# Performance work log

Measured on AMD Instinct MI355X. Metric: run time of the kernel, lower is better.

## Reference

```python
import jax, jax.numpy as jnp
import numpy as np

EPS = 1e-5
HID = 32
FUSED = 33 * 33 * 33  # 35937


def _subnet(x, gamma, beta, W1, b1, W2, b2, W3, b3):
    # BatchNorm1d in training mode: batch mean / biased variance
    mu = jnp.mean(x, axis=0)
    var = jnp.mean((x - mu) ** 2, axis=0)
    xn = (x - mu) / jnp.sqrt(var + EPS) * gamma + beta
    h = jax.nn.relu(xn @ W1 + b1)
    h = jax.nn.relu(h @ W2 + b2)
    return jax.nn.relu(h @ W3 + b3)


def _subnet_params(key, in_dim):
    ks = jax.random.split(key, 6)
    s_in = 1.0 / np.sqrt(in_dim)
    s_h = 1.0 / np.sqrt(HID)
    return dict(
        gamma=jnp.ones((in_dim,), jnp.float32),
        beta=jnp.zeros((in_dim,), jnp.float32),
        W1=jax.random.uniform(ks[0], (in_dim, HID), jnp.float32, -s_in, s_in),
        b1=jax.random.uniform(ks[1], (HID,), jnp.float32, -s_in, s_in),
        W2=jax.random.uniform(ks[2], (HID, HID), jnp.float32, -s_h, s_h),
        b2=jax.random.uniform(ks[3], (HID,), jnp.float32, -s_h, s_h),
        W3=jax.random.uniform(ks[4], (HID, HID), jnp.float32, -s_h, s_h),
        b3=jax.random.uniform(ks[5], (HID,), jnp.float32, -s_h, s_h),
    )


def setup_inputs() -> dict:
    key = jax.random.key(0)
    ks = jax.random.split(key, 10)
    B = 8192
    inp = {
        'US_x': jax.random.normal(ks[0], (B, 1024), jnp.float32),
        'CDFI_x': jax.random.normal(ks[1], (B, 1024), jnp.float32),
        'marker_x': jax.random.normal(ks[2], (B, 10), jnp.float32),
    }
    for pref, k, d in (('us', ks[3], 1024), ('cd', ks[4], 1024), ('mk', ks[5], 10)):
        for n, v in _subnet_params(k, d).items():
            inp[f'{pref}_{n}'] = v
    s1 = 1.0 / np.sqrt(FUSED)
    s2 = 1.0 / np.sqrt(33)
    inp['Wf1'] = jax.random.uniform(ks[6], (FUSED, 33), jnp.float32, -s1, s1)
    inp['bf1'] = jax.random.uniform(ks[7], (33,), jnp.float32, -s1, s1)
    inp['Wf2'] = jax.random.uniform(ks[8], (33, 5), jnp.float32, -s2, s2)
    inp['bf2'] = jax.random.uniform(ks[9], (5,), jnp.float32, -s2, s2)
    return inp


def reference(US_x, CDFI_x, marker_x,
              us_gamma, us_beta, us_W1, us_b1, us_W2, us_b2, us_W3, us_b3,
              cd_gamma, cd_beta, cd_W1, cd_b1, cd_W2, cd_b2, cd_W3, cd_b3,
              mk_gamma, mk_beta, mk_W1, mk_b1, mk_W2, mk_b2, mk_W3, mk_b3,
              Wf1, bf1, Wf2, bf2):
    B = US_x.shape[0]
    us_h = _subnet(US_x, us_gamma, us_beta, us_W1, us_b1, us_W2, us_b2, us_W3, us_b3)
    cd_h = _subnet(CDFI_x, cd_gamma, cd_beta, cd_W1, cd_b1, cd_W2, cd_b2, cd_W3, cd_b3)
    mk_h = _subnet(marker_x, mk_gamma, mk_beta, mk_W1, mk_b1, mk_W2, mk_b2, mk_W3, mk_b3)
    ones = jnp.ones((B, 1), jnp.float32)
    us1 = jnp.concatenate([ones, us_h], axis=1)   # [B,33]
    cd1 = jnp.concatenate([ones, cd_h], axis=1)   # [B,33]
    mk1 = jnp.concatenate([ones, mk_h], axis=1)   # [B,33]
    # fused[b,k,j,i] = mk1[b,k] * cd1[b,j] * us1[b,i]; flattened row-major
    fused = jnp.einsum('bk,bj,bi->bkji', mk1, cd1, us1).reshape(B, FUSED)
    h = jax.nn.relu(fused @ Wf1 + bf1)
    return jax.nn.sigmoid(h @ Wf2 + bf2)
```

## Files before the change

kernel.cpp:

```cpp
#include <hip/hip_runtime.h>
#include <hip/hip_bf16.h>
#include <math.h>

typedef __hip_bfloat16 bf16;
typedef __attribute__((ext_vector_type(4))) float f32x4;
typedef __attribute__((ext_vector_type(8))) short s16x8;

#define NB 8192
#define KP 1152
#define NP 1152
#define NK 36
#define SBLK 256

struct SubP {
    const float* x; const float* gamma; const float* beta;
    const float* W1; const float* b1; const float* W2; const float* b2;
    const float* W3; const float* b3;
    float* sum; float* sumsq; float* a; float* b1p; float* hout;
    int F;
};
struct SubP3 { SubP s[3]; };

__global__ void __launch_bounds__(256) stats3_kernel(SubP3 P) {
    const SubP p = P.s[blockIdx.z];
    int t = threadIdx.x;
    int blk = blockIdx.x;
    int row0 = blk * 32;
    if (p.F == 1024) {
        f32x4 s = {0.f, 0.f, 0.f, 0.f}, s2 = {0.f, 0.f, 0.f, 0.f};
        const float* xp = p.x + (size_t)row0 * 1024 + t * 4;
        #pragma unroll 8
        for (int r = 0; r < 32; r++) {
            f32x4 v = *(const f32x4*)(xp + (size_t)r * 1024);
            s += v; s2 += v * v;
        }
        int f = t * 4;
        *(f32x4*)&p.sum[(size_t)blk * 2048 + f]   = s;
        *(f32x4*)&p.sumsq[(size_t)blk * 2048 + f] = s2;
    } else {
        __shared__ float ls[16], ls2[16];
        if (t < 16) { ls[t] = 0.f; ls2[t] = 0.f; }
        __syncthreads();
        int F = p.F;
        for (int idx = t; idx < 32 * F; idx += 256) {
            float v = p.x[(size_t)row0 * F + idx];
            int f = idx % 10;
            atomicAdd(&ls[f], v);
            atomicAdd(&ls2[f], v * v);
        }
        __syncthreads();
        if (t < F) {
            p.sum[(size_t)blk * 2048 + t]   = ls[t];
            p.sumsq[(size_t)blk * 2048 + t] = ls2[t];
        }
    }
}

__global__ void prep3_kernel(SubP3 P) {
    const SubP p = P.s[blockIdx.y];
    int f0 = blockIdx.x * 32;
    if (f0 >= p.F) return;
    int t = threadIdx.x;
    __shared__ float c_sh[32];
    __shared__ float red[8][33];
    __shared__ float rs[8][33], rs2[8][33];
    int fc = p.F - f0; if (fc > 32) fc = 32;
    int fi = t & 31, g = t >> 5;
    {
        float s = 0.f, s2 = 0.f;
        if (fi < fc) {
            for (int blk = g; blk < SBLK; blk += 8) {
                s  += p.sum[(size_t)blk * 2048 + f0 + fi];
                s2 += p.sumsq[(size_t)blk * 2048 + f0 + fi];
            }
        }
        rs[g][fi] = s; rs2[g][fi] = s2;
    }
    __syncthreads();
    if (t < 32) {
        float c = 0.f;
        if (t < fc) {
            float sm = 0.f, sq = 0.f;
            #pragma unroll
            for (int gg = 0; gg < 8; gg++) { sm += rs[gg][t]; sq += rs2[gg][t]; }
            int f = f0 + t;
            float mu  = sm * (1.f / 8192.f);
            float var = sq * (1.f / 8192.f) - mu * mu;
            float a = p.gamma[f] * rsqrtf(var + 1e-5f);
            p.a[f] = a;
            c = p.beta[f] - mu * a;
        }
        c_sh[t] = c;
    }
    __syncthreads();
    int h = t & 31; g = t >> 5;
    float s = 0.f;
    for (int fi2 = g; fi2 < fc; fi2 += 8)
        s += c_sh[fi2] * p.W1[(size_t)(f0 + fi2) * 32 + h];
    red[g][h] = s;
    __syncthreads();
    if (t < 32) {
        float tot = 0.f;
        #pragma unroll
        for (int gg = 0; gg < 8; gg++) tot += red[gg][t];
        atomicAdd(&p.b1p[t], tot);
    }
}

__global__ void __launch_bounds__(256) subnet3_kernel(SubP3 P) {
    const SubP p = P.s[blockIdx.y];
    const int F = p.F;
    __shared__ float smem[8832];
    float* Red = smem;
    float* H1  = smem + 3456;
    float* W23 = smem + 4608;
    float* H2  = smem;

    int t = threadIdx.x;
    int row0 = blockIdx.x * 32;
    int kg = t >> 6;
    int lane = t & 63;
    int hg = lane & 7, h0 = hg * 4;
    int rg = (lane >> 3) & 3;
    int ks = lane >> 5;

    float acc[4][8] = {};

    if (F == 1024) {
        float* Xt = smem;
        float* Wt = smem + 4224;
        int xr = t >> 3, xc = (t & 7) * 16;
        int wk = t >> 1, wh = (t & 1) * 16;
        const float* xbase = p.x + (size_t)row0 * 1024;
        f32x4 xp[4], wp[4]; float av;
        #pragma unroll
        for (int i = 0; i < 4; i++) xp[i] = *(const f32x4*)&xbase[(size_t)xr * 1024 + xc + i * 4];
        #pragma unroll
        for (int i = 0; i < 4; i++) wp[i] = *(const f32x4*)&p.W1[(size_t)wk * 32 + wh + i * 4];
        av = p.a[wk];
        int kb = (kg * 2 + ks) * 16;
        for (int c = 0; c < 8; c++) {
            __syncthreads();
            #pragma unroll
            for (int i = 0; i < 4; i++) *(f32x4*)&Xt[xr * 132 + xc + i * 4] = xp[i];
            #pragma unroll
            for (int i = 0; i < 4; i++) *(f32x4*)&Wt[wk * 36 + wh + i * 4] = wp[i] * av;
            if (c < 7) {
                int k0 = (c + 1) * 128;
                #pragma unroll
                for (int i = 0; i < 4; i++) xp[i] = *(const f32x4*)&xbase[(size_t)xr * 1024 + k0 + xc + i * 4];
                #pragma unroll
                for (int i = 0; i < 4; i++) wp[i] = *(const f32x4*)&p.W1[(size_t)(k0 + wk) * 32 + wh + i * 4];
                av = p.a[k0 + wk];
            }
            __syncthreads();
            #pragma unroll
            for (int s = 0; s < 4; s++) {
                int kk = kb + s * 4;
                f32x4 wv[4], xv[8];
                #pragma unroll
                for (int j = 0; j < 4; j++)  wv[j]  = *(const f32x4*)&Wt[(kk + j) * 36 + h0];
                #pragma unroll
                for (int ri = 0; ri < 8; ri++) xv[ri] = *(const f32x4*)&Xt[(rg + 4 * ri) * 132 + kk];
                #pragma unroll
                for (int j = 0; j < 4; j++)
                    #pragma unroll
                    for (int hi = 0; hi < 4; hi++) {
                        float w = wv[j][hi];
                        #pragma unroll
                        for (int ri = 0; ri < 8; ri++)
                            acc[hi][ri] = fmaf(w, xv[ri][j], acc[hi][ri]);
                    }
            }
        }
    } else {
        float* Xt = smem;
        float* Wt = smem + 2176;
        int kbase = (kg * 2 + ks) * 8;
        for (int k0 = 0; k0 < F; k0 += 64) {
            int kc = F - k0; if (kc > 64) kc = 64;
            int kcp = (kc + 3) & ~3;
            __syncthreads();
            for (int idx = t; idx < 32 * kcp; idx += 256) {
                int r = idx / kcp, kk = idx - r * kcp;
                Xt[r * 68 + kk] = (kk < kc) ? p.x[(size_t)(row0 + r) * F + k0 + kk] : 0.f;
            }
            for (int idx = t; idx < kcp * 32; idx += 256) {
                int kk = idx >> 5, hh = idx & 31;
                Wt[kk * 36 + hh] = (kk < kc) ? p.a[k0 + kk] * p.W1[(size_t)(k0 + kk) * 32 + hh] : 0.f;
            }
            __syncthreads();
            #pragma unroll
            for (int s = 0; s < 2; s++) {
                int kk = kbase + s * 4;
                if (kk < kcp) {
                    f32x4 wv[4], xv[8];
                    #pragma unroll
                    for (int j = 0; j < 4; j++)  wv[j]  = *(const f32x4*)&Wt[(kk + j) * 36 + h0];
                    #pragma unroll
                    for (int ri = 0; ri < 8; ri++) xv[ri] = *(const f32x4*)&Xt[(rg + 4 * ri) * 68 + kk];
                    #pragma unroll
                    for (int j = 0; j < 4; j++)
                        #pragma unroll
                        for (int hi = 0; hi < 4; hi++) {
                            float w = wv[j][hi];
                            #pragma unroll
                            for (int ri = 0; ri < 8; ri++)
                                acc[hi][ri] = fmaf(w, xv[ri][j], acc[hi][ri]);
                        }
                }
            }
        }
    }
    #pragma unroll
    for (int hi = 0; hi < 4; hi++)
        #pragma unroll
        for (int ri = 0; ri < 8; ri++)
            acc[hi][ri] += __shfl_xor(acc[hi][ri], 32);
    __syncthreads();
    if (kg > 0 && ks == 0) {
        #pragma unroll
        for (int ri = 0; ri < 8; ri++) {
            int r = rg + 4 * ri;
            f32x4 v = {acc[0][ri], acc[1][ri], acc[2][ri], acc[3][ri]};
            *(f32x4*)&Red[(kg - 1) * 1152 + r * 36 + h0] = v;
        }
    }
    for (int idx = t; idx < 1024; idx += 256) W23[(idx >> 5) * 33 + (idx & 31)] = p.W2[idx];
    __syncthreads();
    if (kg == 0 && ks == 0) {
        f32x4 b;
        #pragma unroll
        for (int hi = 0; hi < 4; hi++) b[hi] = p.b1[h0 + hi] + p.b1p[h0 + hi];
        #pragma unroll
        for (int ri = 0; ri < 8; ri++) {
            int r = rg + 4 * ri;
            f32x4 v = {acc[0][ri], acc[1][ri], acc[2][ri], acc[3][ri]};
            #pragma unroll
            for (int pp = 0; pp < 3; pp++)
                v += *(const f32x4*)&Red[pp * 1152 + r * 36 + h0];
            v += b;
            #pragma unroll
            for (int hi = 0; hi < 4; hi++)
                H1[r * 36 + h0 + hi] = fmaxf(v[hi], 0.f);
        }
    }
    __syncthreads();
    int h = t & 31, rq = t >> 5;
    {
        float a2[4] = {};
        for (int q = 0; q < 32; q++) {
            float w = W23[q * 33 + h];
            #pragma unroll
            for (int i = 0; i < 4; i++) a2[i] += H1[(rq * 4 + i) * 36 + q] * w;
        }
        float bv = p.b2[h];
        #pragma unroll
        for (int i = 0; i < 4; i++) H2[(rq * 4 + i) * 36 + h] = fmaxf(a2[i] + bv, 0.f);
    }
    __syncthreads();
    for (int idx = t; idx < 1024; idx += 256) W23[(idx >> 5) * 33 + (idx & 31)] = p.W3[idx];
    __syncthreads();
    {
        float a3[4] = {};
        for (int q = 0; q < 32; q++) {
            float w = W23[q * 33 + h];
            #pragma unroll
            for (int i = 0; i < 4; i++) a3[i] += H2[(rq * 4 + i) * 36 + q] * w;
        }
        float bv = p.b3[h];
        #pragma unroll
        for (int i = 0; i < 4; i++)
            p.hout[(size_t)(row0 + rq * 4 + i) * 32 + h] = fmaxf(a3[i] + bv, 0.f);
    }
}

__global__ void __launch_bounds__(256) build_both(const float* __restrict__ mk_h,
                           const float* __restrict__ us_h,
                           bf16* __restrict__ p1,
                           const float* __restrict__ Wf1, bf16* __restrict__ W2t) {
    int blk = blockIdx.x;
    int t = threadIdx.x;
    if (blk < NB / 4) {
        int r = t >> 6, lane = t & 63;
        int b = blk * 4 + r;
        __shared__ float mk1[4][34], us1[4][34];
        if (lane == 0) { mk1[r][0] = 1.f; us1[r][0] = 1.f; }
        if (lane < 32) mk1[r][lane + 1] = mk_h[(size_t)b * 32 + lane];
        else           us1[r][lane - 31] = us_h[(size_t)b * 32 + (lane - 32)];
        __syncthreads();
        #pragma unroll
        for (int c = 0; c < 3; c++) {
            int chunk = lane + 64 * c;
            if (chunk < 144) {
                int base = chunk * 8;
                s16x8 v;
                #pragma unroll
                for (int e = 0; e < 8; e++) {
                    int idx = base + e;
                    float val = 0.f;
                    if (idx < 1089) {
                        int k = idx / 33, i = idx - k * 33;
                        val = mk1[r][k] * us1[r][i];
                    }
                    __hip_bfloat16 hb = __float2bfloat16(val);
                    v[e] = *(short*)&hb;
                }
                *(s16x8*)(p1 + (size_t)b * KP + base) = v;
            }
        }
    } else {
        int kj = blk - NB / 4;
        int k = kj / 33, j = kj - k * 33;
        __shared__ float tile[1089];
        const float* src = Wf1 + (size_t)k * 35937 + (size_t)j * 1089;
        for (int idx = t; idx < 1089; idx += 256) tile[idx] = src[idx];
        __syncthreads();
        for (int idx = t; idx < 1089; idx += 256) {
            int o = idx / 33, i = idx - o * 33;
            W2t[(size_t)(j * 33 + o) * KP + k * 33 + i] = __float2bfloat16(tile[i * 33 + o]);
        }
        if (k == 0) {
            bf16 z = __float2bfloat16(0.f);
            for (int idx = t; idx < 33 * 63; idx += 256) {
                int o = idx / 63, kkp = 1089 + idx - o * 63;
                W2t[(size_t)(j * 33 + o) * KP + kkp] = z;
            }
        }
    }
}

__global__ void __launch_bounds__(256) gemm_kernel(const bf16* __restrict__ A,
                                                   const bf16* __restrict__ Bt,
                                                   bf16* __restrict__ S) {
    __shared__ __align__(16) bf16 As[2][128 * 32];
    __shared__ __align__(16) bf16 Bs[2][128 * 32];
    int t = threadIdx.x;
    int m0 = blockIdx.x * 128;
    int n0 = blockIdx.y * 128;
    int wave = t >> 6, lane = t & 63;
    int wm = (wave & 1) * 64, wn = (wave >> 1) * 64;
    int fr = lane & 15;
    int q  = lane >> 4;
    int rsw = (fr >> 1) & 3;

    int lr = lane >> 2;
    int sslot = (lane & 3) ^ ((lane >> 3) & 3);
    const bf16* Ag = A  + (size_t)(m0 + wave * 32 + lr) * KP + sslot * 8;
    const bf16* Bg = Bt + (size_t)(n0 + wave * 32 + lr) * KP + sslot * 8;

    f32x4 acc[4][4] = {};

    auto stage = [&](int buf, int k0) {
        bf16* Ad = &As[buf][wave * 1024];
        bf16* Bd = &Bs[buf][wave * 1024];
        __builtin_amdgcn_global_load_lds(
            (const __attribute__((address_space(1))) void*)(Ag + k0),
            (__attribute__((address_space(3))) void*)(Ad), 16, 0, 0);
        __builtin_amdgcn_global_load_lds(
            (const __attribute__((address_space(1))) void*)(Ag + k0 + (size_t)16 * KP),
            (__attribute__((address_space(3))) void*)(Ad + 16 * 32), 16, 0, 0);
        __builtin_amdgcn_global_load_lds(
            (const __attribute__((address_space(1))) void*)(Bg + k0),
            (__attribute__((address_space(3))) void*)(Bd), 16, 0, 0);
        __builtin_amdgcn_global_load_lds(
            (const __attribute__((address_space(1))) void*)(Bg + k0 + (size_t)16 * KP),
            (__attribute__((address_space(3))) void*)(Bd + 16 * 32), 16, 0, 0);
    };

    stage(0, 0);
    __syncthreads();
    int cur = 0;
    for (int ks = 0; ks < NK; ks++) {
        if (ks < NK - 1) stage(cur ^ 1, (ks + 1) * 32);
        const bf16* Ab = &As[cur][0];
        const bf16* Bb = &Bs[cur][0];
        s16x8 bfr[4];
        #pragma unroll
        for (int nt = 0; nt < 4; nt++) {
            int row = wn + nt * 16 + fr;
            bfr[nt] = *(const s16x8*)(Bb + row * 32 + ((q ^ rsw) * 8));
        }
        #pragma unroll
        for (int mt = 0; mt < 4; mt++) {
            int row = wm + mt * 16 + fr;
            s16x8 af = *(const s16x8*)(Ab + row * 32 + ((q ^ rsw) * 8));
            #pragma unroll
            for (int nt = 0; nt < 4; nt++)
                acc[mt][nt] = __builtin_amdgcn_mfma_f32_16x16x32_bf16(af, bfr[nt], acc[mt][nt], 0, 0, 0);
        }
        __syncthreads();
        cur ^= 1;
    }
    int col = lane & 15, rowg = (lane >> 4) * 4;
    #pragma unroll
    for (int mt = 0; mt < 4; mt++)
        #pragma unroll
        for (int nt = 0; nt < 4; nt++)
            #pragma unroll
            for (int r = 0; r < 4; r++) {
                int gr = m0 + wm + mt * 16 + rowg + r;
                int gc = n0 + wn + nt * 16 + col;
                S[(size_t)gr * NP + gc] = __float2bfloat16(acc[mt][nt][r]);
            }
}

__global__ void __launch_bounds__(256) epilogue_kernel(const bf16* __restrict__ S,
                                const float* __restrict__ cd_h,
                                const float* __restrict__ bf1, const float* __restrict__ Wf2,
                                const float* __restrict__ bf2, float* __restrict__ out) {
    int w = threadIdx.x >> 6;
    int lane = threadIdx.x & 63;
    int b = blockIdx.x * 4 + w;
    __shared__ __align__(16) unsigned short Sl[4][1152];
    __shared__ float cdsh[4][33];
    __shared__ float hsh[4][40];
    const bf16* Srow = S + (size_t)b * NP;
    #pragma unroll
    for (int pass = 0; pass < 3; pass++) {
        int idx = lane + pass * 64;
        if (idx < 144)
            *(s16x8*)&Sl[w][idx * 8] = *(const s16x8*)(Srow + idx * 8);
    }
    if (lane == 0) cdsh[w][0] = 1.f;
    if (lane < 32) cdsh[w][lane + 1] = cd_h[(size_t)b * 32 + lane];
    __syncthreads();
    if (lane < 33) {
        float acc = bf1[lane];
        #pragma unroll 3
        for (int j = 0; j < 33; j++) {
            unsigned short sv = Sl[w][j * 33 + lane];
            acc += cdsh[w][j] * __bfloat162float(*(bf16*)&sv);
        }
        hsh[w][lane] = fmaxf(acc, 0.f);
    }
    __syncthreads();
    if (lane < 5) {
        float o = bf2[lane];
        for (int q = 0; q < 33; q++) o += hsh[w][q] * Wf2[q * 5 + lane];
        out[(size_t)b * 5 + lane] = 1.f / (1.f + expf(-o));
    }
}

extern "C" void kernel_launch(void* const* d_in, const int* in_sizes, int n_in,
                              void* d_out, int out_size, void* d_ws, size_t ws_size,
                              hipStream_t stream) {
    const float* US_x     = (const float*)d_in[0];
    const float* CDFI_x   = (const float*)d_in[1];
    const float* marker_x = (const float*)d_in[2];
    const float* Wf1      = (const float*)d_in[27];
    const float* bf1      = (const float*)d_in[28];
    const float* Wf2      = (const float*)d_in[29];
    const float* bf2      = (const float*)d_in[30];
    float* out = (float*)d_out;

    char* ws = (char*)d_ws;
    size_t off = 0;
    auto alloc = [&](size_t bytes) -> void* {
        void* p = ws + off;
        off = (off + bytes + 255) & ~(size_t)255;
        return p;
    };

    float* b1p_buf  = (float*)alloc(3 * 128 * sizeof(float));
    float* pstat    = (float*)alloc((size_t)3 * SBLK * 2048 * sizeof(float));
    float* a_buf[3], *h_buf[3];
    for (int i = 0; i < 3; i++) {
        a_buf[i] = (float*)alloc(1024 * 4);
        h_buf[i] = (float*)alloc((size_t)NB * 32 * 4);
    }
    bf16*  p1   = (bf16*)alloc((size_t)NB * KP * 2);
    bf16*  W2t  = (bf16*)alloc((size_t)NP * KP * 2);
    bf16*  S    = (bf16*)alloc((size_t)NB * NP * 2);

    SubP3 P;
    const float* xs[3] = {US_x, CDFI_x, marker_x};
    int Fs[3] = {1024, 1024, 10};
    for (int i = 0; i < 3; i++) {
        int base = 3 + i * 8;
        P.s[i].x     = xs[i];
        P.s[i].gamma = (const float*)d_in[base + 0];
        P.s[i].beta  = (const float*)d_in[base + 1];
        P.s[i].W1    = (const float*)d_in[base + 2];
        P.s[i].b1    = (const float*)d_in[base + 3];
        P.s[i].W2    = (const float*)d_in[base + 4];
        P.s[i].b2    = (const float*)d_in[base + 5];
        P.s[i].W3    = (const float*)d_in[base + 6];
        P.s[i].b3    = (const float*)d_in[base + 7];
        P.s[i].sum   = pstat + (size_t)i * SBLK * 2048;
        P.s[i].sumsq = pstat + (size_t)i * SBLK * 2048 + 1024;
        P.s[i].b1p   = b1p_buf + i * 128;
        P.s[i].a     = a_buf[i];
        P.s[i].hout  = h_buf[i];
        P.s[i].F     = Fs[i];
    }

    float* us_h = h_buf[0];
    float* cd_h = h_buf[1];
    float* mk_h = h_buf[2];

    hipMemsetAsync(b1p_buf, 0, 3 * 128 * sizeof(float), stream);

    stats3_kernel<<<dim3(SBLK, 1, 3), 256, 0, stream>>>(P);
    prep3_kernel<<<dim3(32, 3), 256, 0, stream>>>(P);
    subnet3_kernel<<<dim3(256, 3), 256, 0, stream>>>(P);

    build_both<<<NB / 4 + 1089, 256, 0, stream>>>(mk_h, us_h, p1, Wf1, W2t);

    gemm_kernel<<<dim3(NB / 128, NP / 128), 256, 0, stream>>>(p1, W2t, S);

    epilogue_kernel<<<NB / 4, 256, 0, stream>>>(S, cd_h, bf1, Wf2, bf2, out);
}
```

Baseline: 255.0 us.

## Restructure bf16 GEMM to 256x144 tiles with 8 waves and split-phase prefetch

The GEMM block tile grows from 128x128 with 4 waves to 256x144 with 8 waves, and the K step from 32 to 64. Each wave now owns 32 rows across all 144 columns, so every loaded B fragment is reused over two A fragments. The next A tile is prefetched before the first K half and the next B tile between the two halves, with explicit vmcnt waits and raw barriers in place of __syncthreads. MFMA sections run at raised s_setprio. This gives more reuse per LDS load and fewer barriers, at the cost of 112KB of LDS (one block per CU) and heavier register use from 18 accumulators plus 9 B fragments.

Measured after the change: 246.4 us. -3.4%, faster.

```diff
diff --git a/kernel.cpp b/kernel.cpp
--- a/kernel.cpp
+++ b/kernel.cpp
@@ -9,7 +9,7 @@
 #define NB 8192
 #define KP 1152
 #define NP 1152
-#define NK 36
+#define NKT 18
 #define SBLK 256
 
 struct SubP {
@@ -330,78 +330,108 @@
     }
 }
 
-__global__ void __launch_bounds__(256) gemm_kernel(const bf16* __restrict__ A,
+__global__ void __launch_bounds__(512) gemm_kernel(const bf16* __restrict__ A,
                                                    const bf16* __restrict__ Bt,
                                                    bf16* __restrict__ S) {
-    __shared__ __align__(16) bf16 As[2][128 * 32];
-    __shared__ __align__(16) bf16 Bs[2][128 * 32];
+    __shared__ __align__(16) bf16 As[2][256 * 64];
+    __shared__ __align__(16) bf16 Bs[2][192 * 64];
     int t = threadIdx.x;
-    int m0 = blockIdx.x * 128;
-    int n0 = blockIdx.y * 128;
-    int wave = t >> 6, lane = t & 63;
-    int wm = (wave & 1) * 64, wn = (wave >> 1) * 64;
+    int wv = t >> 6, lane = t & 63;
+    int m0 = blockIdx.x * 256;
+    int n0 = blockIdx.y * 144;
     int fr = lane & 15;
     int q  = lane >> 4;
-    int rsw = (fr >> 1) & 3;
-
-    int lr = lane >> 2;
-    int sslot = (lane & 3) ^ ((lane >> 3) & 3);
-    const bf16* Ag = A  + (size_t)(m0 + wave * 32 + lr) * KP + sslot * 8;
-    const bf16* Bg = Bt + (size_t)(n0 + wave * 32 + lr) * KP + sslot * 8;
-
-    f32x4 acc[4][4] = {};
-
-    auto stage = [&](int buf, int k0) {
-        bf16* Ad = &As[buf][wave * 1024];
-        bf16* Bd = &Bs[buf][wave * 1024];
-        __builtin_amdgcn_global_load_lds(
-            (const __attribute__((address_space(1))) void*)(Ag + k0),
-            (__attribute__((address_space(3))) void*)(Ad), 16, 0, 0);
-        __builtin_amdgcn_global_load_lds(
-            (const __attribute__((address_space(1))) void*)(Ag + k0 + (size_t)16 * KP),
-            (__attribute__((address_space(3))) void*)(Ad + 16 * 32), 16, 0, 0);
-        __builtin_amdgcn_global_load_lds(
-            (const __attribute__((address_space(1))) void*)(Bg + k0),
-            (__attribute__((address_space(3))) void*)(Bd), 16, 0, 0);
-        __builtin_amdgcn_global_load_lds(
-            (const __attribute__((address_space(1))) void*)(Bg + k0 + (size_t)16 * KP),
-            (__attribute__((address_space(3))) void*)(Bd + 16 * 32), 16, 0, 0);
+    int lr8 = lane >> 3;
+    int sslot = (lane & 7) ^ lr8;
+
+    const bf16* Ag = A  + (size_t)(m0 + wv * 32 + lr8) * KP + sslot * 8;
+    const bf16* Bg = Bt + (size_t)(n0 + wv * 24 + lr8) * KP + sslot * 8;
+
+    f32x4 acc[2][9] = {};
+
+    auto stageA = [&](int buf, int T) {
+        bf16* Ad = &As[buf][wv * 32 * 64];
+        const bf16* s = Ag + T * 64;
+        #pragma unroll
+        for (int i = 0; i < 4; i++)
+            __builtin_amdgcn_global_load_lds(
+                (const __attribute__((address_space(1))) void*)(s + (size_t)i * 8 * KP),
+                (__attribute__((address_space(3))) void*)(Ad + i * 512), 16, 0, 0);
     };
-
-    stage(0, 0);
-    __syncthreads();
-    int cur = 0;
-    for (int ks = 0; ks < NK; ks++) {
-        if (ks < NK - 1) stage(cur ^ 1, (ks + 1) * 32);
-        const bf16* Ab = &As[cur][0];
-        const bf16* Bb = &Bs[cur][0];
-        s16x8 bfr[4];
-        #pragma unroll
-        for (int nt = 0; nt < 4; nt++) {
-            int row = wn + nt * 16 + fr;
-            bfr[nt] = *(const s16x8*)(Bb + row * 32 + ((q ^ rsw) * 8));
-        }
-        #pragma unroll
-        for (int mt = 0; mt < 4; mt++) {
-            int row = wm + mt * 16 + fr;
-            s16x8 af = *(const s16x8*)(Ab + row * 32 + ((q ^ rsw) * 8));
-            #pragma unroll
-            for (int nt = 0; nt < 4; nt++)
-                acc[mt][nt] = __builtin_amdgcn_mfma_f32_16x16x32_bf16(af, bfr[nt], acc[mt][nt], 0, 0, 0);
-        }
-        __syncthreads();
-        cur ^= 1;
-    }
+    auto stageB = [&](int buf, int T) {
+        bf16* Bd = &Bs[buf][wv * 24 * 64];
+        const bf16* s = Bg + T * 64;
+        #pragma unroll
+        for (int c = 0; c < 3; c++)
+            __builtin_amdgcn_global_load_lds(
+                (const __attribute__((address_space(1))) void*)(s + (size_t)c * 8 * KP),
+                (__attribute__((address_space(3))) void*)(Bd + c * 512), 16, 0, 0);
+    };
+
+    stageA(0, 0);
+    stageB(0, 0);
+
+    for (int T = 0; T < NKT; T++) {
+        int b = T & 1;
+        const bf16* Ab = &As[b][0];
+        const bf16* Bb = &Bs[b][0];
+        if (T < NKT - 1) {
+            stageA(b ^ 1, T + 1);
+            asm volatile("s_waitcnt vmcnt(4)" ::: "memory");
+        } else {
+            asm volatile("s_waitcnt vmcnt(0)" ::: "memory");
+        }
+        __builtin_amdgcn_s_barrier();
+        asm volatile("" ::: "memory");
+        {
+            int sl = (q ^ (fr & 7)) * 8;
+            s16x8 af0 = *(const s16x8*)(Ab + (wv * 32 + fr) * 64 + sl);
+            s16x8 af1 = *(const s16x8*)(Ab + (wv * 32 + 16 + fr) * 64 + sl);
+            s16x8 bfv[9];
+            #pragma unroll
+            for (int n2 = 0; n2 < 9; n2++)
+                bfv[n2] = *(const s16x8*)(Bb + (n2 * 16 + fr) * 64 + sl);
+            __builtin_amdgcn_s_setprio(1);
+            #pragma unroll
+            for (int n2 = 0; n2 < 9; n2++) {
+                acc[0][n2] = __builtin_amdgcn_mfma_f32_16x16x32_bf16(af0, bfv[n2], acc[0][n2], 0, 0, 0);
+                acc[1][n2] = __builtin_amdgcn_mfma_f32_16x16x32_bf16(af1, bfv[n2], acc[1][n2], 0, 0, 0);
+            }
+            __builtin_amdgcn_s_setprio(0);
+        }
+        if (T < NKT - 1) stageB(b ^ 1, T + 1);
+        {
+            int sl = ((4 + q) ^ (fr & 7)) * 8;
+            s16x8 af0 = *(const s16x8*)(Ab + (wv * 32 + fr) * 64 + sl);
+            s16x8 af1 = *(const s16x8*)(Ab + (wv * 32 + 16 + fr) * 64 + sl);
+            s16x8 bfv[9];
+            #pragma unroll
+            for (int n2 = 0; n2 < 9; n2++)
+                bfv[n2] = *(const s16x8*)(Bb + (n2 * 16 + fr) * 64 + sl);
+            __builtin_amdgcn_s_setprio(1);
+            #pragma unroll
+            for (int n2 = 0; n2 < 9; n2++) {
+                acc[0][n2] = __builtin_amdgcn_mfma_f32_16x16x32_bf16(af0, bfv[n2], acc[0][n2], 0, 0, 0);
+                acc[1][n2] = __builtin_amdgcn_mfma_f32_16x16x32_bf16(af1, bfv[n2], acc[1][n2], 0, 0, 0);
+            }
+            __builtin_amdgcn_s_setprio(0);
+        }
+        asm volatile("s_waitcnt lgkmcnt(0)" ::: "memory");
+        __builtin_amdgcn_sched_barrier(0);
+        __builtin_amdgcn_s_barrier();
+        asm volatile("" ::: "memory");
+    }
+
     int col = lane & 15, rowg = (lane >> 4) * 4;
     #pragma unroll
-    for (int mt = 0; mt < 4; mt++)
-        #pragma unroll
-        for (int nt = 0; nt < 4; nt++)
+    for (int mt = 0; mt < 2; mt++)
+        #pragma unroll
+        for (int n2 = 0; n2 < 9; n2++)
             #pragma unroll
             for (int r = 0; r < 4; r++) {
-                int gr = m0 + wm + mt * 16 + rowg + r;
-                int gc = n0 + wn + nt * 16 + col;
-                S[(size_t)gr * NP + gc] = __float2bfloat16(acc[mt][nt][r]);
+                int gr = m0 + wv * 32 + mt * 16 + rowg + r;
+                int gc = n0 + n2 * 16 + col;
+                S[(size_t)gr * NP + gc] = __float2bfloat16(acc[mt][n2][r]);
             }
 }
 
@@ -507,7 +537,7 @@
 
     build_both<<<NB / 4 + 1089, 256, 0, stream>>>(mk_h, us_h, p1, Wf1, W2t);
 
-    gemm_kernel<<<dim3(NB / 128, NP / 128), 256, 0, stream>>>(p1, W2t, S);
+    gemm_kernel<<<dim3(NB / 256, NP / 144), 512, 0, stream>>>(p1, W2t, S);
 
     epilogue_kernel<<<NB / 4, 256, 0, stream>>>(S, cd_h, bf1, Wf2, bf2, out);
 }
```
